# Optimization experiments

Hardware: AMD Instinct MI355X
Metric: run time of the kernel (lower is better)

Reference implementation:

```python
import jax, jax.numpy as jnp
import numpy as np

# BitLinear follows the BitNet b1.58 recipe used by fla's HGRN-Bit:
#   x -> RMSNorm(no weight) -> per-token int8 activation quant (STE)
#   w -> ternary quant with global mean-abs scale (STE)
#   out = x_q @ w_q.T

def _rms_norm(x, eps=1e-8, weight=None):
    var = jnp.mean(x * x, axis=-1, keepdims=True)
    y = x * jax.lax.rsqrt(var + eps)
    return y * weight if weight is not None else y


def _act_quant(x):
    # per-token absmax int8 quant-dequant with straight-through estimator
    scale = 127.0 / jnp.clip(jnp.max(jnp.abs(x), axis=-1, keepdims=True), 1e-5, None)
    q = jnp.clip(jnp.round(x * scale), -128, 127) / scale
    return x + jax.lax.stop_gradient(q - x)


def _weight_quant(w):
    # ternary {-1,0,1} quant-dequant with global mean-abs scale, STE
    scale = 1.0 / jnp.clip(jnp.mean(jnp.abs(w)), 1e-5, None)
    q = jnp.clip(jnp.round(w * scale), -1, 1) / scale
    return w + jax.lax.stop_gradient(q - w)


def _bit_linear(x, w):
    xq = _act_quant(_rms_norm(x))
    wq = _weight_quant(w)
    return jnp.einsum('...i,oi->...o', xq, wq)


def setup_inputs() -> dict:
    key = jax.random.key(0)
    ks = jax.random.split(key, 5)
    B, S = 2, 4096
    D_IN = 4096           # input_dim == 2 * hidden_size
    H = 2048              # hidden_size
    INTER = 2 * H         # HGRNBitMLP intermediate_size = hidden_size*2 = 4096
    condition = jax.random.normal(ks[0], (B, S, D_IN), dtype=jnp.float32)
    w_gate = jax.random.normal(ks[1], (2 * INTER, D_IN), dtype=jnp.float32) * 0.02   # [8192,4096]
    w_down = jax.random.normal(ks[2], (D_IN, INTER), dtype=jnp.float32) * 0.02        # [4096,4096]
    norm_weight = jnp.ones((2 * H,), dtype=jnp.float32)                                # RMSNorm(hidden_size*2)
    w_out = jax.random.normal(ks[3], (2 * H, 2 * H), dtype=jnp.float32) * 0.02         # [4096,4096]
    return {"condition": condition, "w_gate": w_gate, "w_down": w_down,
            "norm_weight": norm_weight, "w_out": w_out}


def reference(condition, w_gate, w_down, norm_weight, w_out):
    # HGRNBitMLP: gate_proj -> chunk -> swiglu -> down_proj
    y = _bit_linear(condition, w_gate)              # [B,S,8192]
    gate, v = jnp.split(y, 2, axis=-1)              # each [B,S,4096]
    h = _bit_linear(gate * jax.nn.sigmoid(gate) * v, w_down)  # swiglu then down, [B,S,4096]
    # AdaLN head: RMSNorm (learned weight) then quantized out projection
    h = _rms_norm(h, eps=1e-6, weight=norm_weight)
    params = _bit_linear(h, w_out)                  # [B,S,4096]
    scale, shift = jnp.split(params, 2, axis=-1)    # each [B,S,2048]
    return (scale, shift)
```

## Files before the change

kernel.cpp:

```cpp
#include <hip/hip_runtime.h>
#include <hip/hip_bf16.h>

typedef float f32x4 __attribute__((ext_vector_type(4)));
typedef short bf16x8 __attribute__((ext_vector_type(8)));
typedef unsigned short u16;


__device__ __forceinline__ void gload_lds16(const void* g, void* l) {
  __builtin_amdgcn_global_load_lds(
      (const __attribute__((address_space(1))) unsigned int*)g,
      (__attribute__((address_space(3))) unsigned int*)l, 16, 0, 0);
}

__device__ __forceinline__ u16 f2bf(float f) {
  unsigned u = __builtin_bit_cast(unsigned, f);
  u += 0x7fffu + ((u >> 16) & 1u);
  return (u16)(u >> 16);
}

__device__ __forceinline__ float wmean_clip(const double* p, double cnt) {
  double m = *p / cnt;
  if (m < 1e-5) m = 1e-5;
  return (float)m;
}

__device__ __forceinline__ float blk_sum(float v, float* s4) {
  for (int m = 32; m; m >>= 1) v += __shfl_xor(v, m);
  if ((threadIdx.x & 63) == 0) s4[threadIdx.x >> 6] = v;
  __syncthreads();
  float r = s4[0] + s4[1] + s4[2] + s4[3];
  __syncthreads();
  return r;
}

__device__ __forceinline__ float blk_max(float v, float* s4) {
  for (int m = 32; m; m >>= 1) v = fmaxf(v, __shfl_xor(v, m));
  if ((threadIdx.x & 63) == 0) s4[threadIdx.x >> 6] = v;
  __syncthreads();
  float r = fmaxf(fmaxf(s4[0], s4[1]), fmaxf(s4[2], s4[3]));
  __syncthreads();
  return r;
}


__global__ __launch_bounds__(256) void wabs_reduce(
    const float* __restrict__ W, size_t n4, double* __restrict__ out) {
  __shared__ double s4[4];
  const float4* W4 = (const float4*)W;
  size_t i = (size_t)blockIdx.x * 256 + threadIdx.x;
  size_t stride = (size_t)gridDim.x * 256;
  double s = 0.0;
  for (; i < n4; i += stride) {
    float4 v = W4[i];
    s += (double)fabsf(v.x);
    s += (double)fabsf(v.y);
    s += (double)fabsf(v.z);
    s += (double)fabsf(v.w);
  }
  for (int m = 32; m; m >>= 1) s += __shfl_xor(s, m);
  if ((threadIdx.x & 63) == 0) s4[threadIdx.x >> 6] = s;
  __syncthreads();
  if (threadIdx.x == 0) atomicAdd(out, s4[0] + s4[1] + s4[2] + s4[3]);
}


__global__ __launch_bounds__(256) void wquant(
    const float* __restrict__ W, u16* __restrict__ Wq, size_t n4,
    const double* __restrict__ sum, double cnt) {
  float cm = wmean_clip(sum, cnt);
  float scale = 1.0f / cm;
  const float4* W4 = (const float4*)W;
  size_t i = (size_t)blockIdx.x * 256 + threadIdx.x;
  size_t stride = (size_t)gridDim.x * 256;
  for (; i < n4; i += stride) {
    float4 v = W4[i];
    ushort4 o;
    o.x = f2bf(fminf(fmaxf(rintf(v.x * scale), -1.f), 1.f));
    o.y = f2bf(fminf(fmaxf(rintf(v.y * scale), -1.f), 1.f));
    o.z = f2bf(fminf(fmaxf(rintf(v.z * scale), -1.f), 1.f));
    o.w = f2bf(fminf(fmaxf(rintf(v.w * scale), -1.f), 1.f));
    *(ushort4*)&Wq[i * 4] = o;
  }
}


template <bool HEAD>
__global__ __launch_bounds__(256) void rowquant(
    const float* __restrict__ X, const float* __restrict__ nw,
    u16* __restrict__ Aq, float* __restrict__ rowscale, float eps1) {
  __shared__ float s4[4];
  const int t = threadIdx.x;
  const size_t base = (size_t)blockIdx.x * 4096;
  float x[16];
#pragma unroll
  for (int c = 0; c < 4; ++c) {
    float4 v = *(const float4*)&X[base + c * 1024 + t * 4];
    x[c * 4 + 0] = v.x; x[c * 4 + 1] = v.y;
    x[c * 4 + 2] = v.z; x[c * 4 + 3] = v.w;
  }
  float ss = 0.f;
#pragma unroll
  for (int i = 0; i < 16; ++i) ss += x[i] * x[i];
  ss = blk_sum(ss, s4);
  float inv = 1.0f / sqrtf(ss * (1.0f / 4096.0f) + eps1);
  if (HEAD) {
#pragma unroll
    for (int c = 0; c < 4; ++c) {
      float4 w = *(const float4*)&nw[c * 1024 + t * 4];
      x[c * 4 + 0] = x[c * 4 + 0] * inv * w.x;
      x[c * 4 + 1] = x[c * 4 + 1] * inv * w.y;
      x[c * 4 + 2] = x[c * 4 + 2] * inv * w.z;
      x[c * 4 + 3] = x[c * 4 + 3] * inv * w.w;
    }
    float ss2 = 0.f;
#pragma unroll
    for (int i = 0; i < 16; ++i) ss2 += x[i] * x[i];
    ss2 = blk_sum(ss2, s4);
    inv = 1.0f / sqrtf(ss2 * (1.0f / 4096.0f) + 1e-8f);
  }
#pragma unroll
  for (int i = 0; i < 16; ++i) x[i] = x[i] * inv;
  float amax = 0.f;
#pragma unroll
  for (int i = 0; i < 16; ++i) amax = fmaxf(amax, fabsf(x[i]));
  amax = blk_max(amax, s4);
  float cs = fmaxf(amax, 1e-5f);
  float sx = 127.0f / cs;
#pragma unroll
  for (int c = 0; c < 4; ++c) {
    ushort4 o;
    float q0 = fminf(fmaxf(rintf(x[c * 4 + 0] * sx), -128.f), 127.f);
    float q1 = fminf(fmaxf(rintf(x[c * 4 + 1] * sx), -128.f), 127.f);
    float q2 = fminf(fmaxf(rintf(x[c * 4 + 2] * sx), -128.f), 127.f);
    float q3 = fminf(fmaxf(rintf(x[c * 4 + 3] * sx), -128.f), 127.f);
    o.x = f2bf(q0); o.y = f2bf(q1); o.z = f2bf(q2); o.w = f2bf(q3);
    *(ushort4*)&Aq[base + c * 1024 + t * 4] = o;
  }
  if (t == 0) rowscale[blockIdx.x] = cs / 127.0f;
}


__global__ __launch_bounds__(256) void gemm1_fused(
    const u16* __restrict__ A, const u16* __restrict__ Wg,
    float* __restrict__ SW, const float* __restrict__ rowscale,
    const double* __restrict__ wsum) {
  const int K = 4096;
  __shared__ u16 As[128 * 32];
  __shared__ u16 Bg[64 * 32];
  __shared__ u16 Bv[64 * 32];
  const int t = threadIdx.x;
  const int bm0 = blockIdx.y * 128;
  const int bn0 = blockIdx.x * 64;
  const int lane = t & 63, wave = t >> 6;
  const int wr = wave >> 1, wc = wave & 1;

  f32x4 accg[4][2] = {};
  f32x4 accv[4][2] = {};

  const int srow = t >> 2, scol = (t & 3) * 8;
  const u16* ga0 = A + (size_t)(bm0 + srow) * K + scol;
  const u16* ga1 = ga0 + (size_t)64 * K;
  const u16* gg = Wg + (size_t)(bn0 + srow) * K + scol;
  const u16* gv = Wg + (size_t)(4096 + bn0 + srow) * K + scol;
  u16* lA0 = As + t * 8;
  u16* lA1 = As + 2048 + t * 8;
  u16* lG = Bg + t * 8;
  u16* lV = Bv + t * 8;

  for (int kt = 0; kt < K; kt += 32) {
    gload_lds16(ga0 + kt, lA0);
    gload_lds16(ga1 + kt, lA1);
    gload_lds16(gg + kt, lG);
    gload_lds16(gv + kt, lV);
    __syncthreads();
    const int ar = wr * 64 + (lane & 15);
    const int br = wc * 32 + (lane & 15);
    const int ch = (lane >> 4) * 8;
    bf16x8 af[4], bg[2], bv[2];
#pragma unroll
    for (int m = 0; m < 4; ++m) af[m] = *(const bf16x8*)&As[(ar + m * 16) * 32 + ch];
#pragma unroll
    for (int n = 0; n < 2; ++n) {
      bg[n] = *(const bf16x8*)&Bg[(br + n * 16) * 32 + ch];
      bv[n] = *(const bf16x8*)&Bv[(br + n * 16) * 32 + ch];
    }
#pragma unroll
    for (int m = 0; m < 4; ++m)
#pragma unroll
      for (int n = 0; n < 2; ++n) {
        accg[m][n] = __builtin_amdgcn_mfma_f32_16x16x32_bf16(af[m], bg[n], accg[m][n], 0, 0, 0);
        accv[m][n] = __builtin_amdgcn_mfma_f32_16x16x32_bf16(af[m], bv[n], accv[m][n], 0, 0, 0);
      }
    __syncthreads();
  }

  const float cm = wmean_clip(wsum, 33554432.0);
#pragma unroll
  for (int m = 0; m < 4; ++m) {
    const int r0 = bm0 + wr * 64 + m * 16 + (lane >> 4) * 4;
#pragma unroll
    for (int j = 0; j < 4; ++j) {
      const int row = r0 + j;
      const float f = rowscale[row] * cm;
#pragma unroll
      for (int n = 0; n < 2; ++n) {
        const int col = bn0 + wc * 32 + n * 16 + (lane & 15);
        float g = accg[m][n][j] * f;
        float v = accv[m][n][j] * f;
        float s = g / (1.0f + expf(-g)) * v;
        SW[(size_t)row * 4096 + col] = s;
      }
    }
  }
}


template <int EPI>
__global__ __launch_bounds__(256) void gemm_bt(
    const u16* __restrict__ A, const u16* __restrict__ B,
    float* __restrict__ C, const float* __restrict__ rowscale,
    const double* __restrict__ wsum, double wcnt, int M) {
  const int K = 4096, N = 4096;
  __shared__ u16 As[128 * 32];
  __shared__ u16 Bs[128 * 32];
  const int t = threadIdx.x;
  const int bm0 = blockIdx.y * 128, bn0 = blockIdx.x * 128;
  const int lane = t & 63, wave = t >> 6;
  const int wr = wave >> 1, wc = wave & 1;

  f32x4 acc[4][4] = {};

  const int srow = t >> 2, scol = (t & 3) * 8;
  const u16* gA0 = A + (size_t)(bm0 + srow) * K + scol;
  const u16* gA1 = gA0 + (size_t)64 * K;
  const u16* gB0 = B + (size_t)(bn0 + srow) * K + scol;
  const u16* gB1 = gB0 + (size_t)64 * K;
  u16* lA0 = As + t * 8;
  u16* lA1 = As + 2048 + t * 8;
  u16* lB0 = Bs + t * 8;
  u16* lB1 = Bs + 2048 + t * 8;

  for (int kt = 0; kt < K; kt += 32) {
    gload_lds16(gA0 + kt, lA0);
    gload_lds16(gA1 + kt, lA1);
    gload_lds16(gB0 + kt, lB0);
    gload_lds16(gB1 + kt, lB1);
    __syncthreads();
    const int ar = wr * 64 + (lane & 15);
    const int br = wc * 64 + (lane & 15);
    const int ch = (lane >> 4) * 8;
    bf16x8 af[4], bf[4];
#pragma unroll
    for (int m = 0; m < 4; ++m) af[m] = *(const bf16x8*)&As[(ar + m * 16) * 32 + ch];
#pragma unroll
    for (int n = 0; n < 4; ++n) bf[n] = *(const bf16x8*)&Bs[(br + n * 16) * 32 + ch];
#pragma unroll
    for (int m = 0; m < 4; ++m)
#pragma unroll
      for (int n = 0; n < 4; ++n)
        acc[m][n] = __builtin_amdgcn_mfma_f32_16x16x32_bf16(af[m], bf[n], acc[m][n], 0, 0, 0);
    __syncthreads();
  }

  const float cm = wmean_clip(wsum, wcnt);
#pragma unroll
  for (int m = 0; m < 4; ++m) {
    const int r0 = bm0 + wr * 64 + m * 16 + (lane >> 4) * 4;
#pragma unroll
    for (int j = 0; j < 4; ++j) {
      const int row = r0 + j;
      const float f = rowscale[row] * cm;
#pragma unroll
      for (int n = 0; n < 4; ++n) {
        const int col = bn0 + wc * 64 + n * 16 + (lane & 15);
        const float val = acc[m][n][j] * f;
        if (EPI == 0) {
          C[(size_t)row * N + col] = val;
        } else {
          if (col < 2048)
            C[(size_t)row * 2048 + col] = val;
          else
            C[(size_t)M * 2048 + (size_t)row * 2048 + (col - 2048)] = val;
        }
      }
    }
  }
}


extern "C" void kernel_launch(void* const* d_in, const int* in_sizes, int n_in,
                              void* d_out, int out_size, void* d_ws, size_t ws_size,
                              hipStream_t stream) {
  const float* cond = (const float*)d_in[0];
  const float* w_gate = (const float*)d_in[1];
  const float* w_down = (const float*)d_in[2];
  const float* norm_w = (const float*)d_in[3];
  const float* w_out = (const float*)d_in[4];
  float* out = (float*)d_out;

  const int M = in_sizes[0] / 4096;

  char* ws = (char*)d_ws;
  double* sums = (double*)ws;
  u16* wq_gate = (u16*)(ws + 256);
  u16* wq_down = wq_gate + (size_t)8192 * 4096;
  u16* wq_out = wq_down + (size_t)4096 * 4096;
  u16* Aq = wq_out + (size_t)4096 * 4096;
  float* rowscale = (float*)(Aq + (size_t)M * 4096);
  float* act = rowscale + 8192;

  hipMemsetAsync(sums, 0, 3 * sizeof(double), stream);

  wabs_reduce<<<1024, 256, 0, stream>>>(w_gate, (size_t)8192 * 4096 / 4, &sums[0]);
  wabs_reduce<<<1024, 256, 0, stream>>>(w_down, (size_t)4096 * 4096 / 4, &sums[1]);
  wabs_reduce<<<1024, 256, 0, stream>>>(w_out, (size_t)4096 * 4096 / 4, &sums[2]);

  wquant<<<2048, 256, 0, stream>>>(w_gate, wq_gate, (size_t)8192 * 4096 / 4, &sums[0], 33554432.0);
  wquant<<<2048, 256, 0, stream>>>(w_down, wq_down, (size_t)4096 * 4096 / 4, &sums[1], 16777216.0);
  wquant<<<2048, 256, 0, stream>>>(w_out, wq_out, (size_t)4096 * 4096 / 4, &sums[2], 16777216.0);

  rowquant<false><<<M, 256, 0, stream>>>(cond, nullptr, Aq, rowscale, 1e-8f);
  gemm1_fused<<<dim3(4096 / 64, M / 128), 256, 0, stream>>>(Aq, wq_gate, act, rowscale, &sums[0]);

  rowquant<false><<<M, 256, 0, stream>>>(act, nullptr, Aq, rowscale, 1e-8f);
  gemm_bt<0><<<dim3(4096 / 128, M / 128), 256, 0, stream>>>(Aq, wq_down, act, rowscale, &sums[1], 16777216.0, M);

  rowquant<true><<<M, 256, 0, stream>>>(act, norm_w, Aq, rowscale, 1e-6f);
  gemm_bt<1><<<dim3(4096 / 128, M / 128), 256, 0, stream>>>(Aq, wq_out, out, rowscale, &sums[2], 16777216.0, M);
}
```

Baseline: 1.793 ms.

## Switch quantized GEMMs from bf16 to int8 MFMA with XCD-aware tile swizzle

Stores quantized weights and activations as int8 instead of bf16 and runs all three GEMMs with i32 16x16x64 int8 MFMA, doubling K per tile step and halving operand bytes. The shared-memory layout is changed to k-chunk-major 16-byte rows to match the int8 fragment shape. It also remaps workgroup indices so that neighbouring tiles land on the same XCD for better L2 reuse. Results stay exact because the values are small integers accumulated in int32.

```diff
diff --git a/kernel.cpp b/kernel.cpp
--- a/kernel.cpp
+++ b/kernel.cpp
@@ -1,9 +1,8 @@
 #include <hip/hip_runtime.h>
 #include <hip/hip_bf16.h>
 
-typedef float f32x4 __attribute__((ext_vector_type(4)));
-typedef short bf16x8 __attribute__((ext_vector_type(8)));
-typedef unsigned short u16;
+typedef int i32x4 __attribute__((ext_vector_type(4)));
+typedef signed char i8;
 
 
 __device__ __forceinline__ void gload_lds16(const void* g, void* l) {
@@ -12,12 +11,6 @@
       (__attribute__((address_space(3))) unsigned int*)l, 16, 0, 0);
 }
 
-__device__ __forceinline__ u16 f2bf(float f) {
-  unsigned u = __builtin_bit_cast(unsigned, f);
-  u += 0x7fffu + ((u >> 16) & 1u);
-  return (u16)(u >> 16);
-}
-
 __device__ __forceinline__ float wmean_clip(const double* p, double cnt) {
   double m = *p / cnt;
   if (m < 1e-5) m = 1e-5;
@@ -40,6 +33,14 @@
   float r = fmaxf(fmaxf(s4[0], s4[1]), fmaxf(s4[2], s4[3]));
   __syncthreads();
   return r;
+}
+
+__device__ __forceinline__ void xcd_swz(int gx, int& bm, int& bn) {
+  const int nwg = gx * gridDim.y;
+  const int o = blockIdx.y * gx + blockIdx.x;
+  const int s = (o & 7) * (nwg >> 3) + (o >> 3);
+  bm = s / gx;
+  bn = s % gx;
 }
 
 
@@ -65,7 +66,7 @@
 
 
 __global__ __launch_bounds__(256) void wquant(
-    const float* __restrict__ W, u16* __restrict__ Wq, size_t n4,
+    const float* __restrict__ W, i8* __restrict__ Wq, size_t n4,
     const double* __restrict__ sum, double cnt) {
   float cm = wmean_clip(sum, cnt);
   float scale = 1.0f / cm;
@@ -74,12 +75,12 @@
   size_t stride = (size_t)gridDim.x * 256;
   for (; i < n4; i += stride) {
     float4 v = W4[i];
-    ushort4 o;
-    o.x = f2bf(fminf(fmaxf(rintf(v.x * scale), -1.f), 1.f));
-    o.y = f2bf(fminf(fmaxf(rintf(v.y * scale), -1.f), 1.f));
-    o.z = f2bf(fminf(fmaxf(rintf(v.z * scale), -1.f), 1.f));
-    o.w = f2bf(fminf(fmaxf(rintf(v.w * scale), -1.f), 1.f));
-    *(ushort4*)&Wq[i * 4] = o;
+    char4 o;
+    o.x = (i8)fminf(fmaxf(rintf(v.x * scale), -1.f), 1.f);
+    o.y = (i8)fminf(fmaxf(rintf(v.y * scale), -1.f), 1.f);
+    o.z = (i8)fminf(fmaxf(rintf(v.z * scale), -1.f), 1.f);
+    o.w = (i8)fminf(fmaxf(rintf(v.w * scale), -1.f), 1.f);
+    *(char4*)&Wq[i * 4] = o;
   }
 }
 
@@ -87,7 +88,7 @@
 template <bool HEAD>
 __global__ __launch_bounds__(256) void rowquant(
     const float* __restrict__ X, const float* __restrict__ nw,
-    u16* __restrict__ Aq, float* __restrict__ rowscale, float eps1) {
+    i8* __restrict__ Aq, float* __restrict__ rowscale, float eps1) {
   __shared__ float s4[4];
   const int t = threadIdx.x;
   const size_t base = (size_t)blockIdx.x * 4096;
@@ -128,68 +129,67 @@
   float sx = 127.0f / cs;
 #pragma unroll
   for (int c = 0; c < 4; ++c) {
-    ushort4 o;
-    float q0 = fminf(fmaxf(rintf(x[c * 4 + 0] * sx), -128.f), 127.f);
-    float q1 = fminf(fmaxf(rintf(x[c * 4 + 1] * sx), -128.f), 127.f);
-    float q2 = fminf(fmaxf(rintf(x[c * 4 + 2] * sx), -128.f), 127.f);
-    float q3 = fminf(fmaxf(rintf(x[c * 4 + 3] * sx), -128.f), 127.f);
-    o.x = f2bf(q0); o.y = f2bf(q1); o.z = f2bf(q2); o.w = f2bf(q3);
-    *(ushort4*)&Aq[base + c * 1024 + t * 4] = o;
+    char4 o;
+    o.x = (i8)fminf(fmaxf(rintf(x[c * 4 + 0] * sx), -128.f), 127.f);
+    o.y = (i8)fminf(fmaxf(rintf(x[c * 4 + 1] * sx), -128.f), 127.f);
+    o.z = (i8)fminf(fmaxf(rintf(x[c * 4 + 2] * sx), -128.f), 127.f);
+    o.w = (i8)fminf(fmaxf(rintf(x[c * 4 + 3] * sx), -128.f), 127.f);
+    *(char4*)&Aq[base + c * 1024 + t * 4] = o;
   }
   if (t == 0) rowscale[blockIdx.x] = cs / 127.0f;
 }
 
 
 __global__ __launch_bounds__(256) void gemm1_fused(
-    const u16* __restrict__ A, const u16* __restrict__ Wg,
+    const i8* __restrict__ A, const i8* __restrict__ Wg,
     float* __restrict__ SW, const float* __restrict__ rowscale,
     const double* __restrict__ wsum) {
   const int K = 4096;
-  __shared__ u16 As[128 * 32];
-  __shared__ u16 Bg[64 * 32];
-  __shared__ u16 Bv[64 * 32];
+  __shared__ i8 As[8192];
+  __shared__ i8 Bg[4096];
+  __shared__ i8 Bv[4096];
   const int t = threadIdx.x;
-  const int bm0 = blockIdx.y * 128;
-  const int bn0 = blockIdx.x * 64;
+  int bmi, bni;
+  xcd_swz(64, bmi, bni);
+  const int bm0 = bmi * 128, bn0 = bni * 64;
   const int lane = t & 63, wave = t >> 6;
   const int wr = wave >> 1, wc = wave & 1;
 
-  f32x4 accg[4][2] = {};
-  f32x4 accv[4][2] = {};
-
-  const int srow = t >> 2, scol = (t & 3) * 8;
-  const u16* ga0 = A + (size_t)(bm0 + srow) * K + scol;
-  const u16* ga1 = ga0 + (size_t)64 * K;
-  const u16* gg = Wg + (size_t)(bn0 + srow) * K + scol;
-  const u16* gv = Wg + (size_t)(4096 + bn0 + srow) * K + scol;
-  u16* lA0 = As + t * 8;
-  u16* lA1 = As + 2048 + t * 8;
-  u16* lG = Bg + t * 8;
-  u16* lV = Bv + t * 8;
-
-  for (int kt = 0; kt < K; kt += 32) {
-    gload_lds16(ga0 + kt, lA0);
-    gload_lds16(ga1 + kt, lA1);
-    gload_lds16(gg + kt, lG);
-    gload_lds16(gv + kt, lV);
+  i32x4 accg[4][2] = {};
+  i32x4 accv[4][2] = {};
+
+  const i8* gA = A + (size_t)(bm0 + (t & 127)) * K + (t >> 7) * 16;
+  const i8* gG = Wg + (size_t)(bn0 + (t & 63)) * K + (t >> 6) * 16;
+  const i8* gV = Wg + (size_t)(4096 + bn0 + (t & 63)) * K + (t >> 6) * 16;
+  i8* lA0 = As + t * 16;
+  i8* lA1 = As + 4096 + t * 16;
+  i8* lG = Bg + t * 16;
+  i8* lV = Bv + t * 16;
+
+  for (int kt = 0; kt < K; kt += 64) {
+    gload_lds16(gA + kt, lA0);
+    gload_lds16(gA + kt + 32, lA1);
+    gload_lds16(gG + kt, lG);
+    gload_lds16(gV + kt, lV);
     __syncthreads();
     const int ar = wr * 64 + (lane & 15);
     const int br = wc * 32 + (lane & 15);
-    const int ch = (lane >> 4) * 8;
-    bf16x8 af[4], bg[2], bv[2];
-#pragma unroll
-    for (int m = 0; m < 4; ++m) af[m] = *(const bf16x8*)&As[(ar + m * 16) * 32 + ch];
+    const int kcA = (lane >> 4) * 2048;
+    const int kcB = (lane >> 4) * 1024;
+    i32x4 af[4], bg[2], bv[2];
+#pragma unroll
+    for (int m = 0; m < 4; ++m) af[m] = *(const i32x4*)&As[kcA + (ar + m * 16) * 16];
 #pragma unroll
     for (int n = 0; n < 2; ++n) {
-      bg[n] = *(const bf16x8*)&Bg[(br + n * 16) * 32 + ch];
-      bv[n] = *(const bf16x8*)&Bv[(br + n * 16) * 32 + ch];
+      bg[n] = *(const i32x4*)&Bg[kcB + (br + n * 16) * 16];
+      bv[n] = *(const i32x4*)&Bv[kcB + (br + n * 16) * 16];
     }
 #pragma unroll
     for (int m = 0; m < 4; ++m)
 #pragma unroll
       for (int n = 0; n < 2; ++n) {
-        accg[m][n] = __builtin_amdgcn_mfma_f32_16x16x32_bf16(af[m], bg[n], accg[m][n], 0, 0, 0);
-        accv[m][n] = __builtin_amdgcn_mfma_f32_16x16x32_bf16(af[m], bv[n], accv[m][n], 0, 0, 0);
+        accg[m][n] = __builtin_amdgcn_mfma_i32_16x16x64_i8(af[m], bg[n], accg[m][n], 0, 0, 0);
+        accv[m][n] = __builtin_amdgcn_mfma_i32_16x16x64_i8(af[m], bv[n], accv[m][n], 0, 0, 0);
       }
     __syncthreads();
   }
@@ -205,8 +205,8 @@
 #pragma unroll
       for (int n = 0; n < 2; ++n) {
         const int col = bn0 + wc * 32 + n * 16 + (lane & 15);
-        float g = accg[m][n][j] * f;
-        float v = accv[m][n][j] * f;
+        float g = (float)accg[m][n][j] * f;
+        float v = (float)accv[m][n][j] * f;
         float s = g / (1.0f + expf(-g)) * v;
         SW[(size_t)row * 4096 + col] = s;
       }
@@ -217,48 +217,47 @@
 
 template <int EPI>
 __global__ __launch_bounds__(256) void gemm_bt(
-    const u16* __restrict__ A, const u16* __restrict__ B,
+    const i8* __restrict__ A, const i8* __restrict__ B,
     float* __restrict__ C, const float* __restrict__ rowscale,
     const double* __restrict__ wsum, double wcnt, int M) {
   const int K = 4096, N = 4096;
-  __shared__ u16 As[128 * 32];
-  __shared__ u16 Bs[128 * 32];
+  __shared__ i8 As[8192];
+  __shared__ i8 Bs[8192];
   const int t = threadIdx.x;
-  const int bm0 = blockIdx.y * 128, bn0 = blockIdx.x * 128;
+  int bmi, bni;
+  xcd_swz(32, bmi, bni);
+  const int bm0 = bmi * 128, bn0 = bni * 128;
   const int lane = t & 63, wave = t >> 6;
   const int wr = wave >> 1, wc = wave & 1;
 
-  f32x4 acc[4][4] = {};
-
-  const int srow = t >> 2, scol = (t & 3) * 8;
-  const u16* gA0 = A + (size_t)(bm0 + srow) * K + scol;
-  const u16* gA1 = gA0 + (size_t)64 * K;
-  const u16* gB0 = B + (size_t)(bn0 + srow) * K + scol;
-  const u16* gB1 = gB0 + (size_t)64 * K;
-  u16* lA0 = As + t * 8;
-  u16* lA1 = As + 2048 + t * 8;
-  u16* lB0 = Bs + t * 8;
-  u16* lB1 = Bs + 2048 + t * 8;
-
-  for (int kt = 0; kt < K; kt += 32) {
-    gload_lds16(gA0 + kt, lA0);
-    gload_lds16(gA1 + kt, lA1);
-    gload_lds16(gB0 + kt, lB0);
-    gload_lds16(gB1 + kt, lB1);
+  i32x4 acc[4][4] = {};
+
+  const i8* gA = A + (size_t)(bm0 + (t & 127)) * K + (t >> 7) * 16;
+  const i8* gB = B + (size_t)(bn0 + (t & 127)) * K + (t >> 7) * 16;
+  i8* lA0 = As + t * 16;
+  i8* lA1 = As + 4096 + t * 16;
+  i8* lB0 = Bs + t * 16;
+  i8* lB1 = Bs + 4096 + t * 16;
+
+  for (int kt = 0; kt < K; kt += 64) {
+    gload_lds16(gA + kt, lA0);
+    gload_lds16(gA + kt + 32, lA1);
+    gload_lds16(gB + kt, lB0);
+    gload_lds16(gB + kt + 32, lB1);
     __syncthreads();
     const int ar = wr * 64 + (lane & 15);
     const int br = wc * 64 + (lane & 15);
-    const int ch = (lane >> 4) * 8;
-    bf16x8 af[4], bf[4];
-#pragma unroll
-    for (int m = 0; m < 4; ++m) af[m] = *(const bf16x8*)&As[(ar + m * 16) * 32 + ch];
-#pragma unroll
-    for (int n = 0; n < 4; ++n) bf[n] = *(const bf16x8*)&Bs[(br + n * 16) * 32 + ch];
+    const int kc = (lane >> 4) * 2048;
+    i32x4 af[4], bfr[4];
+#pragma unroll
+    for (int m = 0; m < 4; ++m) af[m] = *(const i32x4*)&As[kc + (ar + m * 16) * 16];
+#pragma unroll
+    for (int n = 0; n < 4; ++n) bfr[n] = *(const i32x4*)&Bs[kc + (br + n * 16) * 16];
 #pragma unroll
     for (int m = 0; m < 4; ++m)
 #pragma unroll
       for (int n = 0; n < 4; ++n)
-        acc[m][n] = __builtin_amdgcn_mfma_f32_16x16x32_bf16(af[m], bf[n], acc[m][n], 0, 0, 0);
+        acc[m][n] = __builtin_amdgcn_mfma_i32_16x16x64_i8(af[m], bfr[n], acc[m][n], 0, 0, 0);
     __syncthreads();
   }
 
@@ -273,7 +272,7 @@
 #pragma unroll
       for (int n = 0; n < 4; ++n) {
         const int col = bn0 + wc * 64 + n * 16 + (lane & 15);
-        const float val = acc[m][n][j] * f;
+        const float val = (float)acc[m][n][j] * f;
         if (EPI == 0) {
           C[(size_t)row * N + col] = val;
         } else {
@@ -302,10 +301,10 @@
 
   char* ws = (char*)d_ws;
   double* sums = (double*)ws;
-  u16* wq_gate = (u16*)(ws + 256);
-  u16* wq_down = wq_gate + (size_t)8192 * 4096;
-  u16* wq_out = wq_down + (size_t)4096 * 4096;
-  u16* Aq = wq_out + (size_t)4096 * 4096;
+  i8* wq_gate = (i8*)(ws + 256);
+  i8* wq_down = wq_gate + (size_t)8192 * 4096;
+  i8* wq_out = wq_down + (size_t)4096 * 4096;
+  i8* Aq = wq_out + (size_t)4096 * 4096;
   float* rowscale = (float*)(Aq + (size_t)M * 4096);
   float* act = rowscale + 8192;
 
```

Result: faster. 1.630 ms (-9.1%).
